# Optimization experiments

Measured on AMD Instinct MI355X. Metric: run time of the kernel, lower is better.

## Reference

```python
import jax, jax.numpy as jnp
import numpy as np

B, N, D = 2, 2048, 512
H, HD = 8, 64          # nheads, head_dim = D // H
RD = 16                # rl_dim
TEMPER = 1.0
BETA = 1.0
SLOPE = 0.01           # LeakyReLU negative slope
EPS = 1e-5             # LayerNorm eps


def setup_inputs() -> dict:
    key = jax.random.key(0)
    ks = jax.random.split(key, 12)
    s = 0.02
    return {
        "h": jax.random.normal(ks[0], (B, N, D), dtype=jnp.float32),
        "rh": jax.random.normal(ks[1], (B, N, RD), dtype=jnp.float32),
        # weights stored [in, out] (transpose of torch nn.Linear layout); y = x @ W
        "Wl": jax.random.normal(ks[2], (D, H * HD), dtype=jnp.float32) * s,
        "Wr": jax.random.normal(ks[3], (D, H * HD), dtype=jnp.float32) * s,
        "al": jax.random.normal(ks[4], (HD,), dtype=jnp.float32) * s,   # att_l weight
        "ar": jax.random.normal(ks[5], (HD,), dtype=jnp.float32) * s,   # att_r weight
        "Wrs": jax.random.normal(ks[6], (RD, H * RD), dtype=jnp.float32) * s,  # r_source
        "Wrt": jax.random.normal(ks[7], (RD, H * RD), dtype=jnp.float32) * s,  # r_target
        "Wf": jax.random.normal(ks[8], (H * HD, D), dtype=jnp.float32) * s,    # linear_final
        "gamma": jnp.ones((D,), dtype=jnp.float32),
        "beta": jnp.zeros((D,), dtype=jnp.float32),
    }


def _leaky(x):
    return jnp.where(x >= 0, x, SLOPE * x)


def reference(h, rh, Wl, Wr, al, ar, Wrs, Wrt, Wf, gamma, beta):
    # projections -> [B, H, N, HD]
    fl = (h @ Wl).reshape(B, N, H, HD).transpose(0, 2, 1, 3)
    fr = (h @ Wr).reshape(B, N, H, HD).transpose(0, 2, 1, 3)

    # additive GAT-style scores: [B,H,N,1] + [B,H,1,N] -> [B,H,N,N]
    sl = jnp.einsum("bhnd,d->bhn", _leaky(fl), al)
    sr = jnp.einsum("bhnd,d->bhn", _leaky(fr), ar)
    score = sl[:, :, :, None] + sr[:, :, None, :]

    # relational bias: r_k @ r_q -> [B,H,N,N]
    r_k = (rh @ Wrs).reshape(B, N, H, RD).transpose(0, 2, 1, 3)       # [B,H,N,RD]
    r_q = (rh @ Wrt).reshape(B, N, H, RD).transpose(0, 2, 3, 1)       # [B,H,RD,N]
    score = score + BETA * jnp.einsum("bhnr,bhrm->bhnm", r_k, r_q)

    attn = jax.nn.softmax(score / TEMPER, axis=-1)  # dropout1 is identity (eval)

    # weighted sum of fr (note: values are fr, not a separate V)
    context = jnp.einsum("bhnm,bhmd->bhnd", attn, fr)
    h_sa = context.transpose(0, 2, 1, 3).reshape(B, N, H * HD)
    fh = h_sa @ Wf                                   # dropout2 is identity (eval)

    # residual + LayerNorm
    x = h + fh
    mu = jnp.mean(x, axis=-1, keepdims=True)
    var = jnp.var(x, axis=-1, keepdims=True)
    return (x - mu) * jax.lax.rsqrt(var + EPS) * gamma + beta
```

## Files before the change

### kernel.cpp

```cpp
#include <hip/hip_runtime.h>
#include <hip/hip_bf16.h>

typedef __attribute__((ext_vector_type(8))) short short8;
typedef __attribute__((ext_vector_type(4))) float f32x4;
typedef __attribute__((ext_vector_type(4))) unsigned int u32x4;
typedef __attribute__((ext_vector_type(2))) unsigned int u32x2;

#define N_ 2048

__device__ __forceinline__ unsigned short f2bf(float f) {
  return __builtin_bit_cast(unsigned short, __float2bfloat16(f));
}
__device__ __forceinline__ float bf2f(unsigned short u) {
  return __builtin_bit_cast(float, ((unsigned int)u) << 16);
}
__device__ __forceinline__ unsigned int pack2(float lo, float hi) {
  return ((unsigned int)f2bf(hi) << 16) | (unsigned int)f2bf(lo);
}

__global__ __launch_bounds__(256) void k_cast_wT(const float* __restrict__ Wr,
                                                 const float* __restrict__ Wf,
                                                 unsigned short* __restrict__ WrT,
                                                 unsigned short* __restrict__ WfT) {
  const float* W = blockIdx.z ? Wf : Wr;
  unsigned short* WT = blockIdx.z ? WfT : WrT;
  __shared__ float t[32][33];
  const int kt = blockIdx.x * 32, ct = blockIdx.y * 32;
  const int r = threadIdx.x >> 3, c4 = (threadIdx.x & 7) * 4;
  f32x4 v = *reinterpret_cast<const f32x4*>(&W[(kt + r) * 512 + ct + c4]);
#pragma unroll
  for (int j = 0; j < 4; ++j) t[r][c4 + j] = v[j];
  __syncthreads();
  u32x2 o;
  o[0] = pack2(t[c4][r], t[c4 + 1][r]);
  o[1] = pack2(t[c4 + 2][r], t[c4 + 3][r]);
  *reinterpret_cast<u32x2*>(&WT[(ct + r) * 512 + kt + c4]) = o;
}

__global__ __launch_bounds__(256) void k_projr(
    const float* __restrict__ rh, const float* __restrict__ Wrs,
    const float* __restrict__ Wrt,
    unsigned short* __restrict__ rk, unsigned short* __restrict__ rq) {
  const int tid = threadIdx.x;
  const int col = tid & 127;
  const int ro = tid >> 7;
  const int nf = blockIdx.x * 2 + ro;
  const f32x4* src = reinterpret_cast<const f32x4*>(&rh[nf * 16]);
  f32x4 rv[4] = {src[0], src[1], src[2], src[3]};
  float sk = 0.f, sq = 0.f;
#pragma unroll
  for (int k4 = 0; k4 < 4; ++k4)
#pragma unroll
    for (int j = 0; j < 4; ++j) {
      float v = rv[k4][j];
      int k = k4 * 4 + j;
      sk += v * Wrs[k * 128 + col];
      sq += v * Wrt[k * 128 + col];
    }
  int bb = nf >> 11, n = nf & 2047, hh = col >> 4, r = col & 15;
  int oidx = ((bb * 8 + hh) * N_ + n) * 16 + r;
  rk[oidx] = f2bf(sk);
  rq[oidx] = f2bf(sq);
}

__global__ __launch_bounds__(256) void k_proj_fr(
    const float* __restrict__ h, const unsigned short* __restrict__ WrT,
    const float* __restrict__ ar,
    unsigned short* __restrict__ frB, float* __restrict__ sr) {
  const int tid = threadIdx.x;
  const int w = tid >> 6, lane = tid & 63;
  const int c = lane & 15, g = lane >> 4;
  const int rowbase = blockIdx.x * 16;
  const int hh = blockIdx.y * 4 + w;

  f32x4 acc[4];
#pragma unroll
  for (int i = 0; i < 4; ++i) acc[i] = (f32x4){0.f, 0.f, 0.f, 0.f};

#pragma unroll 4
  for (int kt = 0; kt < 512; kt += 32) {
    const float* hp = &h[(rowbase + c) * 512 + kt + 8 * g];
    f32x4 h0 = *reinterpret_cast<const f32x4*>(hp);
    f32x4 h1 = *reinterpret_cast<const f32x4*>(hp + 4);
    u32x4 aw;
    aw[0] = pack2(h0[0], h0[1]);
    aw[1] = pack2(h0[2], h0[3]);
    aw[2] = pack2(h1[0], h1[1]);
    aw[3] = pack2(h1[2], h1[3]);
    short8 a = __builtin_bit_cast(short8, aw);
#pragma unroll
    for (int ht = 0; ht < 4; ++ht) {
      short8 bv = *reinterpret_cast<const short8*>(
          &WrT[(hh * 64 + ht * 16 + c) * 512 + kt + 8 * g]);
      acc[ht] = __builtin_amdgcn_mfma_f32_16x16x32_bf16(a, bv, acc[ht], 0, 0, 0);
    }
  }

  const int b = rowbase >> 11;
  const int bh = b * 8 + hh;
  const int nloc = rowbase & 2047;
  const int jb = nloc >> 5;
  const int t = (nloc >> 4) & 1;

  float arv[4];
#pragma unroll
  for (int ht = 0; ht < 4; ++ht) arv[ht] = ar[ht * 16 + c];

  float ps[4];
#pragma unroll
  for (int r = 0; r < 4; ++r) {
    float s = 0.f;
#pragma unroll
    for (int ht = 0; ht < 4; ++ht) {
      float v = acc[ht][r];
      float lv = v >= 0.f ? v : 0.01f * v;
      s += lv * arv[ht];
    }
    ps[r] = s;
  }
#pragma unroll
  for (int msk = 1; msk < 16; msk <<= 1)
#pragma unroll
    for (int r = 0; r < 4; ++r) ps[r] += __shfl_xor(ps[r], msk);
  if (c == 0) {
#pragma unroll
    for (int r = 0; r < 4; ++r) sr[bh * N_ + nloc + 4 * g + r] = ps[r];
  }
#pragma unroll
  for (int ht = 0; ht < 4; ++ht) {
    int hd = ht * 16 + c;
    u32x2 ov;
    ov[0] = pack2(acc[ht][0], acc[ht][1]);
    ov[1] = pack2(acc[ht][2], acc[ht][3]);
    *reinterpret_cast<u32x2*>(
        &frB[((bh * 64 + jb) * 64 + hd) * 32 + 8 * g + 4 * t]) = ov;
  }
}

__global__ __launch_bounds__(128) void k_attn(
    const unsigned short* __restrict__ rk, const unsigned short* __restrict__ rq,
    const float* __restrict__ sr, const unsigned short* __restrict__ frB,
    unsigned short* __restrict__ O0, unsigned short* __restrict__ O1,
    unsigned short* __restrict__ O2, unsigned short* __restrict__ O3,
    float* __restrict__ lbuf) {
  const int tid = threadIdx.x;
  const int wave = tid >> 6, lane = tid & 63;
  const int c = lane & 15, g = lane >> 4;
  const int bh = blockIdx.y;
  const int b = bh >> 3, hh = bh & 7;
  const int z = blockIdx.z;
  const int qbase = blockIdx.x * 64 + wave * 32;

  short8 brk0 = {0, 0, 0, 0, 0, 0, 0, 0};
  short8 brk1 = {0, 0, 0, 0, 0, 0, 0, 0};
  if (g < 2) {
    brk0 = *reinterpret_cast<const short8*>(&rk[(bh * N_ + qbase + c) * 16 + 8 * g]);
    brk1 = *reinterpret_cast<const short8*>(&rk[(bh * N_ + qbase + 16 + c) * 16 + 8 * g]);
  } else if (g == 2) {
    brk0[0] = (short)0x3F80;
    brk1[0] = (short)0x3F80;
  }

  f32x4 O[2][4];
#pragma unroll
  for (int q = 0; q < 2; ++q)
#pragma unroll
    for (int i = 0; i < 4; ++i) O[q][i] = (f32x4){0.f, 0.f, 0.f, 0.f};
  float lacc0 = 0.f, lacc1 = 0.f;
  const unsigned short* frB_bh = frB + bh * 131072;

  for (int it = 0; it < 4; ++it) {
    const int j0 = z * 512 + it * 128;
    f32x4 S0[8], S1[8];
#pragma unroll
    for (int jh = 0; jh < 8; ++jh) {
      const int jr = j0 + jh * 16 + c;
      short8 a = {0, 0, 0, 0, 0, 0, 0, 0};
      if (g < 2)
        a = *reinterpret_cast<const short8*>(&rq[(bh * N_ + jr) * 16 + 8 * g]);
      else if (g == 2)
        a[0] = (short)f2bf(sr[bh * N_ + jr]);
      f32x4 zz = {0.f, 0.f, 0.f, 0.f};
      S0[jh] = __builtin_amdgcn_mfma_f32_16x16x32_bf16(a, brk0, zz, 0, 0, 0);
      S1[jh] = __builtin_amdgcn_mfma_f32_16x16x32_bf16(a, brk1, zz, 0, 0, 0);
    }
#pragma unroll
    for (int jh = 0; jh < 8; ++jh)
#pragma unroll
      for (int r = 0; r < 4; ++r) {
        float e0 = __expf(S0[jh][r]);
        S0[jh][r] = e0;
        lacc0 += e0;
        float e1 = __expf(S1[jh][r]);
        S1[jh][r] = e1;
        lacc1 += e1;
      }
#pragma unroll
    for (int kk = 0; kk < 4; ++kk) {
      u32x4 p0, p1;
      p0[0] = pack2(S0[2 * kk][0], S0[2 * kk][1]);
      p0[1] = pack2(S0[2 * kk][2], S0[2 * kk][3]);
      p0[2] = pack2(S0[2 * kk + 1][0], S0[2 * kk + 1][1]);
      p0[3] = pack2(S0[2 * kk + 1][2], S0[2 * kk + 1][3]);
      p1[0] = pack2(S1[2 * kk][0], S1[2 * kk][1]);
      p1[1] = pack2(S1[2 * kk][2], S1[2 * kk][3]);
      p1[2] = pack2(S1[2 * kk + 1][0], S1[2 * kk + 1][1]);
      p1[3] = pack2(S1[2 * kk + 1][2], S1[2 * kk + 1][3]);
      short8 pa0 = __builtin_bit_cast(short8, p0);
      short8 pa1 = __builtin_bit_cast(short8, p1);
      const int jb = (j0 >> 5) + kk;
      const unsigned short* fp = frB_bh + jb * 2048 + 8 * g;
#pragma unroll
      for (int ht = 0; ht < 4; ++ht) {
        short8 bv = *reinterpret_cast<const short8*>(fp + (ht * 16 + c) * 32);
        O[0][ht] = __builtin_amdgcn_mfma_f32_16x16x32_bf16(pa0, bv, O[0][ht], 0, 0, 0);
        O[1][ht] = __builtin_amdgcn_mfma_f32_16x16x32_bf16(pa1, bv, O[1][ht], 0, 0, 0);
      }
    }
  }
  lacc0 += __shfl_xor(lacc0, 16);
  lacc0 += __shfl_xor(lacc0, 32);
  lacc1 += __shfl_xor(lacc1, 16);
  lacc1 += __shfl_xor(lacc1, 32);
  if (g == 0) {
    lbuf[(z * 16 + bh) * N_ + qbase + c] = lacc0;
    lbuf[(z * 16 + bh) * N_ + qbase + 16 + c] = lacc1;
  }
  unsigned short* Oz = (z == 0) ? O0 : (z == 1) ? O1 : (z == 2) ? O2 : O3;
#pragma unroll
  for (int q = 0; q < 2; ++q)
#pragma unroll
    for (int ht = 0; ht < 4; ++ht)
#pragma unroll
      for (int r = 0; r < 4; ++r) {
        const int n = qbase + q * 16 + 4 * g + r;
        Oz[(b * N_ + n) * 512 + hh * 64 + ht * 16 + c] = f2bf(O[q][ht][r]);
      }
}

__global__ __launch_bounds__(256) void k_combine(
    const unsigned short* __restrict__ O0, const unsigned short* __restrict__ O1,
    const unsigned short* __restrict__ O2, const unsigned short* __restrict__ O3,
    const float* __restrict__ lbuf, unsigned short* __restrict__ ctx) {
  const int idx = blockIdx.x * 256 + threadIdx.x;
  const int row = idx >> 6;
  const int c8 = (idx & 63) * 8;
  const int b = row >> 11, n = row & 2047;
  const int hh = c8 >> 6;
  const int bh = b * 8 + hh;
  const float denom = lbuf[bh * N_ + n] + lbuf[(16 + bh) * N_ + n] +
                      lbuf[(32 + bh) * N_ + n] + lbuf[(48 + bh) * N_ + n];
  const float inv = 1.f / denom;
  const int off = row * 512 + c8;
  u32x4 v0 = *reinterpret_cast<const u32x4*>(&O0[off]);
  u32x4 v1 = *reinterpret_cast<const u32x4*>(&O1[off]);
  u32x4 v2 = *reinterpret_cast<const u32x4*>(&O2[off]);
  u32x4 v3 = *reinterpret_cast<const u32x4*>(&O3[off]);
  u32x4 ov;
#pragma unroll
  for (int j = 0; j < 4; ++j) {
    float lo = bf2f((unsigned short)(v0[j] & 0xffff)) + bf2f((unsigned short)(v1[j] & 0xffff)) +
               bf2f((unsigned short)(v2[j] & 0xffff)) + bf2f((unsigned short)(v3[j] & 0xffff));
    float hi = bf2f((unsigned short)(v0[j] >> 16)) + bf2f((unsigned short)(v1[j] >> 16)) +
               bf2f((unsigned short)(v2[j] >> 16)) + bf2f((unsigned short)(v3[j] >> 16));
    ov[j] = pack2(lo * inv, hi * inv);
  }
  *reinterpret_cast<u32x4*>(&ctx[off]) = ov;
}

__global__ __launch_bounds__(512) void k_final(
    const unsigned short* __restrict__ ctxB, const unsigned short* __restrict__ WfT,
    const float* __restrict__ h, const float* __restrict__ gamma,
    const float* __restrict__ beta, float* __restrict__ out) {
  __shared__ float red[2][16][9];
  __shared__ float mur[16], rsr[16];
  const int tid = threadIdx.x;
  const int w = tid >> 6, lane = tid & 63;
  const int c = lane & 15, g = lane >> 4;
  const int rowbase = blockIdx.x * 16;

  f32x4 acc[4];
#pragma unroll
  for (int i = 0; i < 4; ++i) acc[i] = (f32x4){0.f, 0.f, 0.f, 0.f};

#pragma unroll 4
  for (int kt = 0; kt < 512; kt += 32) {
    short8 a = *reinterpret_cast<const short8*>(&ctxB[(rowbase + c) * 512 + kt + 8 * g]);
#pragma unroll
    for (int ht = 0; ht < 4; ++ht) {
      short8 bv = *reinterpret_cast<const short8*>(
          &WfT[(w * 64 + ht * 16 + c) * 512 + kt + 8 * g]);
      acc[ht] = __builtin_amdgcn_mfma_f32_16x16x32_bf16(a, bv, acc[ht], 0, 0, 0);
    }
  }
  float x[4][4];
  float px[4], pxx[4];
#pragma unroll
  for (int r = 0; r < 4; ++r) { px[r] = 0.f; pxx[r] = 0.f; }
#pragma unroll
  for (int ht = 0; ht < 4; ++ht)
#pragma unroll
    for (int r = 0; r < 4; ++r) {
      float v = acc[ht][r] + h[(rowbase + 4 * g + r) * 512 + w * 64 + ht * 16 + c];
      x[ht][r] = v;
      px[r] += v;
      pxx[r] += v * v;
    }
#pragma unroll
  for (int msk = 1; msk < 16; msk <<= 1)
#pragma unroll
    for (int r = 0; r < 4; ++r) {
      px[r] += __shfl_xor(px[r], msk);
      pxx[r] += __shfl_xor(pxx[r], msk);
    }
  if (c == 0) {
#pragma unroll
    for (int r = 0; r < 4; ++r) {
      red[0][4 * g + r][w] = px[r];
      red[1][4 * g + r][w] = pxx[r];
    }
  }
  __syncthreads();
  if (tid < 16) {
    float s = 0.f, sq = 0.f;
#pragma unroll
    for (int wv = 0; wv < 8; ++wv) { s += red[0][tid][wv]; sq += red[1][tid][wv]; }
    float mu = s * (1.f / 512.f);
    float var = sq * (1.f / 512.f) - mu * mu;
    mur[tid] = mu;
    rsr[tid] = rsqrtf(var + 1e-5f);
  }
  __syncthreads();
#pragma unroll
  for (int ht = 0; ht < 4; ++ht)
#pragma unroll
    for (int r = 0; r < 4; ++r) {
      const int col = w * 64 + ht * 16 + c;
      const float mu = mur[4 * g + r], rs = rsr[4 * g + r];
      out[(rowbase + 4 * g + r) * 512 + col] =
          (x[ht][r] - mu) * rs * gamma[col] + beta[col];
    }
}

extern "C" void kernel_launch(void* const* d_in, const int* in_sizes, int n_in,
                              void* d_out, int out_size, void* d_ws, size_t ws_size,
                              hipStream_t stream) {
  const float* h     = (const float*)d_in[0];
  const float* rh    = (const float*)d_in[1];
  const float* Wr    = (const float*)d_in[3];
  const float* ar    = (const float*)d_in[5];
  const float* Wrs   = (const float*)d_in[6];
  const float* Wrt   = (const float*)d_in[7];
  const float* Wf    = (const float*)d_in[8];
  const float* gamma = (const float*)d_in[9];
  const float* beta  = (const float*)d_in[10];

  const size_t MB = 1ull << 20;
  char* ws = (char*)d_ws;
  unsigned short* frB  = (unsigned short*)(ws);
  unsigned short* rk   = (unsigned short*)(ws + 4 * MB);
  unsigned short* rq   = (unsigned short*)(ws + 5 * MB);
  float*          sr   = (float*)(ws + 6 * MB);
  float*          lbuf = (float*)(ws + 6 * MB + 256 * 1024);
  unsigned short* WrT  = (unsigned short*)(ws + 6 * MB + 768 * 1024);
  unsigned short* WfT  = (unsigned short*)(ws + 7 * MB + 256 * 1024);
  unsigned short* O0   = (unsigned short*)(ws + 7 * MB + 768 * 1024);
  unsigned short* O1   = (unsigned short*)(ws + 11 * MB + 768 * 1024);
  unsigned short* O2   = (unsigned short*)d_out;
  unsigned short* O3   = (unsigned short*)((char*)d_out + 4 * MB);

  hipLaunchKernelGGL(k_cast_wT, dim3(16, 16, 2), dim3(256), 0, stream, Wr, Wf, WrT, WfT);
  hipLaunchKernelGGL(k_projr, dim3(1024), dim3(256), 0, stream, rh, Wrs, Wrt, rk, rq);
  hipLaunchKernelGGL(k_proj_fr, dim3(256, 2), dim3(256), 0, stream, h, WrT, ar, frB, sr);
  hipLaunchKernelGGL(k_attn, dim3(32, 16, 4), dim3(128), 0, stream, rk, rq, sr, frB,
                     O0, O1, O2, O3, lbuf);
  hipLaunchKernelGGL(k_combine, dim3(1024), dim3(256), 0, stream, O0, O1, O2, O3, lbuf, frB);
  hipLaunchKernelGGL(k_final, dim3(256), dim3(512), 0, stream, frB, WfT, h, gamma, beta,
                     (float*)d_out);
}
```

Baseline: 185.8 us.

## Rewrite attention with 32x32x16 MFMA, permlane32 swaps, and merged prep kernel

The attention kernel now uses single-wave blocks with 32x32x16 bf16 MFMA for both the score and PV products. The sr bias is added in fp32 after the MFMA instead of being folded into the K dimension as a bf16 value, and the probabilities are rearranged into the B-operand layout with permlane32_swap. The fr buffer layout changes to 16-key tiles to match the new operand shape. Output stores become packed 32-bit writes per row. The weight-transpose and r-projection kernels are merged into one launch to save a kernel launch. The risks are lower occupancy from 64-thread blocks and more register pressure from the 16-wide accumulators.

```diff
diff --git a/kernel.cpp b/kernel.cpp
--- a/kernel.cpp
+++ b/kernel.cpp
@@ -3,8 +3,10 @@
 
 typedef __attribute__((ext_vector_type(8))) short short8;
 typedef __attribute__((ext_vector_type(4))) float f32x4;
+typedef __attribute__((ext_vector_type(16))) float f32x16;
 typedef __attribute__((ext_vector_type(4))) unsigned int u32x4;
 typedef __attribute__((ext_vector_type(2))) unsigned int u32x2;
+typedef __attribute__((ext_vector_type(2))) int i32x2;
 
 #define N_ 2048
 
@@ -18,55 +20,57 @@
   return ((unsigned int)f2bf(hi) << 16) | (unsigned int)f2bf(lo);
 }
 
-__global__ __launch_bounds__(256) void k_cast_wT(const float* __restrict__ Wr,
-                                                 const float* __restrict__ Wf,
-                                                 unsigned short* __restrict__ WrT,
-                                                 unsigned short* __restrict__ WfT) {
-  const float* W = blockIdx.z ? Wf : Wr;
-  unsigned short* WT = blockIdx.z ? WfT : WrT;
-  __shared__ float t[32][33];
-  const int kt = blockIdx.x * 32, ct = blockIdx.y * 32;
-  const int r = threadIdx.x >> 3, c4 = (threadIdx.x & 7) * 4;
-  f32x4 v = *reinterpret_cast<const f32x4*>(&W[(kt + r) * 512 + ct + c4]);
-#pragma unroll
-  for (int j = 0; j < 4; ++j) t[r][c4 + j] = v[j];
-  __syncthreads();
-  u32x2 o;
-  o[0] = pack2(t[c4][r], t[c4 + 1][r]);
-  o[1] = pack2(t[c4 + 2][r], t[c4 + 3][r]);
-  *reinterpret_cast<u32x2*>(&WT[(ct + r) * 512 + kt + c4]) = o;
-}
-
-__global__ __launch_bounds__(256) void k_projr(
+__global__ __launch_bounds__(256) void k_prep(
+    const float* __restrict__ Wr, const float* __restrict__ Wf,
     const float* __restrict__ rh, const float* __restrict__ Wrs,
     const float* __restrict__ Wrt,
+    unsigned short* __restrict__ WrT, unsigned short* __restrict__ WfT,
     unsigned short* __restrict__ rk, unsigned short* __restrict__ rq) {
+  __shared__ float t[32][33];
+  const int bid = blockIdx.x;
   const int tid = threadIdx.x;
-  const int col = tid & 127;
-  const int ro = tid >> 7;
-  const int nf = blockIdx.x * 2 + ro;
-  const f32x4* src = reinterpret_cast<const f32x4*>(&rh[nf * 16]);
-  f32x4 rv[4] = {src[0], src[1], src[2], src[3]};
-  float sk = 0.f, sq = 0.f;
-#pragma unroll
-  for (int k4 = 0; k4 < 4; ++k4)
-#pragma unroll
-    for (int j = 0; j < 4; ++j) {
-      float v = rv[k4][j];
-      int k = k4 * 4 + j;
-      sk += v * Wrs[k * 128 + col];
-      sq += v * Wrt[k * 128 + col];
-    }
-  int bb = nf >> 11, n = nf & 2047, hh = col >> 4, r = col & 15;
-  int oidx = ((bb * 8 + hh) * N_ + n) * 16 + r;
-  rk[oidx] = f2bf(sk);
-  rq[oidx] = f2bf(sq);
+  if (bid < 512) {
+    const int zz = bid >> 8, rem = bid & 255;
+    const int kt = (rem & 15) * 32, ct = (rem >> 4) * 32;
+    const float* W = zz ? Wf : Wr;
+    unsigned short* WT = zz ? WfT : WrT;
+    const int r = tid >> 3, c4 = (tid & 7) * 4;
+    f32x4 v = *reinterpret_cast<const f32x4*>(&W[(kt + r) * 512 + ct + c4]);
+#pragma unroll
+    for (int j = 0; j < 4; ++j) t[r][c4 + j] = v[j];
+    __syncthreads();
+    u32x2 o;
+    o[0] = pack2(t[c4][r], t[c4 + 1][r]);
+    o[1] = pack2(t[c4 + 2][r], t[c4 + 3][r]);
+    *reinterpret_cast<u32x2*>(&WT[(ct + r) * 512 + kt + c4]) = o;
+  } else {
+    const int pb = bid - 512;
+    const int col = tid & 127;
+    const int ro = tid >> 7;
+    const int nf = pb * 2 + ro;
+    const f32x4* src = reinterpret_cast<const f32x4*>(&rh[nf * 16]);
+    f32x4 rv[4] = {src[0], src[1], src[2], src[3]};
+    float sk = 0.f, sq = 0.f;
+#pragma unroll
+    for (int k4 = 0; k4 < 4; ++k4)
+#pragma unroll
+      for (int j = 0; j < 4; ++j) {
+        float v = rv[k4][j];
+        int k = k4 * 4 + j;
+        sk += v * Wrs[k * 128 + col];
+        sq += v * Wrt[k * 128 + col];
+      }
+    int bb = nf >> 11, n = nf & 2047, hh = col >> 4, r = col & 15;
+    int oidx = ((bb * 8 + hh) * N_ + n) * 16 + r;
+    rk[oidx] = f2bf(sk);
+    rq[oidx] = f2bf(sq);
+  }
 }
 
 __global__ __launch_bounds__(256) void k_proj_fr(
     const float* __restrict__ h, const unsigned short* __restrict__ WrT,
     const float* __restrict__ ar,
-    unsigned short* __restrict__ frB, float* __restrict__ sr) {
+    unsigned short* __restrict__ frBt, float* __restrict__ sr) {
   const int tid = threadIdx.x;
   const int w = tid >> 6, lane = tid & 63;
   const int c = lane & 15, g = lane >> 4;
@@ -99,8 +103,7 @@
   const int b = rowbase >> 11;
   const int bh = b * 8 + hh;
   const int nloc = rowbase & 2047;
-  const int jb = nloc >> 5;
-  const int t = (nloc >> 4) & 1;
+  const int jb = nloc >> 4;
 
   float arv[4];
 #pragma unroll
@@ -133,109 +136,96 @@
     ov[0] = pack2(acc[ht][0], acc[ht][1]);
     ov[1] = pack2(acc[ht][2], acc[ht][3]);
     *reinterpret_cast<u32x2*>(
-        &frB[((bh * 64 + jb) * 64 + hd) * 32 + 8 * g + 4 * t]) = ov;
-  }
-}
-
-__global__ __launch_bounds__(128) void k_attn(
+        &frBt[(((size_t)bh * 128 + jb) * 64 + hd) * 16 + 4 * g]) = ov;
+  }
+}
+
+__global__ __launch_bounds__(64) void k_attn(
     const unsigned short* __restrict__ rk, const unsigned short* __restrict__ rq,
-    const float* __restrict__ sr, const unsigned short* __restrict__ frB,
+    const float* __restrict__ sr, const unsigned short* __restrict__ frBt,
     unsigned short* __restrict__ O0, unsigned short* __restrict__ O1,
     unsigned short* __restrict__ O2, unsigned short* __restrict__ O3,
     float* __restrict__ lbuf) {
-  const int tid = threadIdx.x;
-  const int wave = tid >> 6, lane = tid & 63;
-  const int c = lane & 15, g = lane >> 4;
-  const int bh = blockIdx.y;
-  const int b = bh >> 3, hh = bh & 7;
+  const int lane = threadIdx.x;
+  const int c5 = lane & 31, hi = lane >> 5;
+  const int bh = blockIdx.y, b = bh >> 3, hh = bh & 7;
   const int z = blockIdx.z;
-  const int qbase = blockIdx.x * 64 + wave * 32;
-
-  short8 brk0 = {0, 0, 0, 0, 0, 0, 0, 0};
-  short8 brk1 = {0, 0, 0, 0, 0, 0, 0, 0};
-  if (g < 2) {
-    brk0 = *reinterpret_cast<const short8*>(&rk[(bh * N_ + qbase + c) * 16 + 8 * g]);
-    brk1 = *reinterpret_cast<const short8*>(&rk[(bh * N_ + qbase + 16 + c) * 16 + 8 * g]);
-  } else if (g == 2) {
-    brk0[0] = (short)0x3F80;
-    brk1[0] = (short)0x3F80;
-  }
-
-  f32x4 O[2][4];
-#pragma unroll
-  for (int q = 0; q < 2; ++q)
-#pragma unroll
-    for (int i = 0; i < 4; ++i) O[q][i] = (f32x4){0.f, 0.f, 0.f, 0.f};
-  float lacc0 = 0.f, lacc1 = 0.f;
-  const unsigned short* frB_bh = frB + bh * 131072;
+  const int qbase = blockIdx.x * 32;
+
+  const short8 brk =
+      *reinterpret_cast<const short8*>(&rk[(bh * N_ + qbase + c5) * 16 + 8 * hi]);
+
+  f32x16 Oa = {0.f, 0.f, 0.f, 0.f, 0.f, 0.f, 0.f, 0.f,
+               0.f, 0.f, 0.f, 0.f, 0.f, 0.f, 0.f, 0.f};
+  f32x16 Ob = Oa;
+  float l = 0.f;
+  const float* sr_bh = sr + bh * N_;
+  const unsigned short* rq_bh = rq + (size_t)bh * N_ * 16;
+  const unsigned short* fb = frBt + (size_t)bh * 128 * 64 * 16;
 
   for (int it = 0; it < 4; ++it) {
     const int j0 = z * 512 + it * 128;
-    f32x4 S0[8], S1[8];
-#pragma unroll
-    for (int jh = 0; jh < 8; ++jh) {
-      const int jr = j0 + jh * 16 + c;
-      short8 a = {0, 0, 0, 0, 0, 0, 0, 0};
-      if (g < 2)
-        a = *reinterpret_cast<const short8*>(&rq[(bh * N_ + jr) * 16 + 8 * g]);
-      else if (g == 2)
-        a[0] = (short)f2bf(sr[bh * N_ + jr]);
-      f32x4 zz = {0.f, 0.f, 0.f, 0.f};
-      S0[jh] = __builtin_amdgcn_mfma_f32_16x16x32_bf16(a, brk0, zz, 0, 0, 0);
-      S1[jh] = __builtin_amdgcn_mfma_f32_16x16x32_bf16(a, brk1, zz, 0, 0, 0);
-    }
-#pragma unroll
-    for (int jh = 0; jh < 8; ++jh)
-#pragma unroll
-      for (int r = 0; r < 4; ++r) {
-        float e0 = __expf(S0[jh][r]);
-        S0[jh][r] = e0;
-        lacc0 += e0;
-        float e1 = __expf(S1[jh][r]);
-        S1[jh][r] = e1;
-        lacc1 += e1;
-      }
-#pragma unroll
-    for (int kk = 0; kk < 4; ++kk) {
-      u32x4 p0, p1;
-      p0[0] = pack2(S0[2 * kk][0], S0[2 * kk][1]);
-      p0[1] = pack2(S0[2 * kk][2], S0[2 * kk][3]);
-      p0[2] = pack2(S0[2 * kk + 1][0], S0[2 * kk + 1][1]);
-      p0[3] = pack2(S0[2 * kk + 1][2], S0[2 * kk + 1][3]);
-      p1[0] = pack2(S1[2 * kk][0], S1[2 * kk][1]);
-      p1[1] = pack2(S1[2 * kk][2], S1[2 * kk][3]);
-      p1[2] = pack2(S1[2 * kk + 1][0], S1[2 * kk + 1][1]);
-      p1[3] = pack2(S1[2 * kk + 1][2], S1[2 * kk + 1][3]);
-      short8 pa0 = __builtin_bit_cast(short8, p0);
-      short8 pa1 = __builtin_bit_cast(short8, p1);
-      const int jb = (j0 >> 5) + kk;
-      const unsigned short* fp = frB_bh + jb * 2048 + 8 * g;
-#pragma unroll
-      for (int ht = 0; ht < 4; ++ht) {
-        short8 bv = *reinterpret_cast<const short8*>(fp + (ht * 16 + c) * 32);
-        O[0][ht] = __builtin_amdgcn_mfma_f32_16x16x32_bf16(pa0, bv, O[0][ht], 0, 0, 0);
-        O[1][ht] = __builtin_amdgcn_mfma_f32_16x16x32_bf16(pa1, bv, O[1][ht], 0, 0, 0);
-      }
-    }
-  }
-  lacc0 += __shfl_xor(lacc0, 16);
-  lacc0 += __shfl_xor(lacc0, 32);
-  lacc1 += __shfl_xor(lacc1, 16);
-  lacc1 += __shfl_xor(lacc1, 32);
-  if (g == 0) {
-    lbuf[(z * 16 + bh) * N_ + qbase + c] = lacc0;
-    lbuf[(z * 16 + bh) * N_ + qbase + 16 + c] = lacc1;
-  }
+#pragma unroll
+    for (int t = 0; t < 4; ++t) {
+      const int jb = j0 + t * 32;
+      short8 a = *reinterpret_cast<const short8*>(&rq_bh[(jb + c5) * 16 + 8 * hi]);
+      f32x16 zz = {0.f, 0.f, 0.f, 0.f, 0.f, 0.f, 0.f, 0.f,
+                   0.f, 0.f, 0.f, 0.f, 0.f, 0.f, 0.f, 0.f};
+      f32x16 S = __builtin_amdgcn_mfma_f32_32x32x16_bf16(a, brk, zz, 0, 0, 0);
+      f32x4 sa = *reinterpret_cast<const f32x4*>(&sr_bh[jb + 4 * hi]);
+      f32x4 sb = *reinterpret_cast<const f32x4*>(&sr_bh[jb + 8 + 4 * hi]);
+      f32x4 sc = *reinterpret_cast<const f32x4*>(&sr_bh[jb + 16 + 4 * hi]);
+      f32x4 sd = *reinterpret_cast<const f32x4*>(&sr_bh[jb + 24 + 4 * hi]);
+      float p[16];
+#pragma unroll
+      for (int r = 0; r < 4; ++r) p[r] = __expf(S[r] + sa[r]);
+#pragma unroll
+      for (int r = 0; r < 4; ++r) p[4 + r] = __expf(S[4 + r] + sb[r]);
+#pragma unroll
+      for (int r = 0; r < 4; ++r) p[8 + r] = __expf(S[8 + r] + sc[r]);
+#pragma unroll
+      for (int r = 0; r < 4; ++r) p[12 + r] = __expf(S[12 + r] + sd[r]);
+#pragma unroll
+      for (int r = 0; r < 16; ++r) l += p[r];
+      int A1 = (int)pack2(p[0], p[1]), B1 = (int)pack2(p[2], p[3]);
+      int C1 = (int)pack2(p[4], p[5]), D1 = (int)pack2(p[6], p[7]);
+      i32x2 r0 = __builtin_amdgcn_permlane32_swap(A1, C1, false, false);
+      i32x2 r1 = __builtin_amdgcn_permlane32_swap(B1, D1, false, false);
+      int A2 = (int)pack2(p[8], p[9]), B2 = (int)pack2(p[10], p[11]);
+      int C2 = (int)pack2(p[12], p[13]), D2 = (int)pack2(p[14], p[15]);
+      i32x2 r2 = __builtin_amdgcn_permlane32_swap(A2, C2, false, false);
+      i32x2 r3 = __builtin_amdgcn_permlane32_swap(B2, D2, false, false);
+      u32x4 f1, f2;
+      f1[0] = (unsigned)r0[0]; f1[1] = (unsigned)r1[0];
+      f1[2] = (unsigned)r0[1]; f1[3] = (unsigned)r1[1];
+      f2[0] = (unsigned)r2[0]; f2[1] = (unsigned)r3[0];
+      f2[2] = (unsigned)r2[1]; f2[3] = (unsigned)r3[1];
+      short8 pb1 = __builtin_bit_cast(short8, f1);
+      short8 pb2 = __builtin_bit_cast(short8, f2);
+      const unsigned short* fp0 = fb + ((size_t)(jb >> 4) * 64) * 16 + 8 * hi;
+      const unsigned short* fp1 = fp0 + 64 * 16;
+      short8 av;
+      av = *reinterpret_cast<const short8*>(fp0 + c5 * 16);
+      Oa = __builtin_amdgcn_mfma_f32_32x32x16_bf16(av, pb1, Oa, 0, 0, 0);
+      av = *reinterpret_cast<const short8*>(fp0 + (32 + c5) * 16);
+      Ob = __builtin_amdgcn_mfma_f32_32x32x16_bf16(av, pb1, Ob, 0, 0, 0);
+      av = *reinterpret_cast<const short8*>(fp1 + c5 * 16);
+      Oa = __builtin_amdgcn_mfma_f32_32x32x16_bf16(av, pb2, Oa, 0, 0, 0);
+      av = *reinterpret_cast<const short8*>(fp1 + (32 + c5) * 16);
+      Ob = __builtin_amdgcn_mfma_f32_32x32x16_bf16(av, pb2, Ob, 0, 0, 0);
+    }
+  }
+  l += __shfl_xor(l, 32);
+  if (hi == 0) lbuf[(z * 16 + bh) * N_ + qbase + c5] = l;
   unsigned short* Oz = (z == 0) ? O0 : (z == 1) ? O1 : (z == 2) ? O2 : O3;
-#pragma unroll
-  for (int q = 0; q < 2; ++q)
-#pragma unroll
-    for (int ht = 0; ht < 4; ++ht)
-#pragma unroll
-      for (int r = 0; r < 4; ++r) {
-        const int n = qbase + q * 16 + 4 * g + r;
-        Oz[(b * N_ + n) * 512 + hh * 64 + ht * 16 + c] = f2bf(O[q][ht][r]);
-      }
+  unsigned int* orow = reinterpret_cast<unsigned int*>(
+      &Oz[((size_t)(b * N_ + qbase + c5)) * 512 + hh * 64]);
+#pragma unroll
+  for (int r = 0; r < 16; r += 2) {
+    const int hd = (r & 3) + 8 * (r >> 2) + 4 * hi;
+    orow[hd >> 1] = pack2(Oa[r], Oa[r + 1]);
+    orow[(32 + hd) >> 1] = pack2(Ob[r], Ob[r + 1]);
+  }
 }
 
 __global__ __launch_bounds__(256) void k_combine(
@@ -357,7 +347,7 @@
 
   const size_t MB = 1ull << 20;
   char* ws = (char*)d_ws;
-  unsigned short* frB  = (unsigned short*)(ws);
+  unsigned short* frBt = (unsigned short*)(ws);
   unsigned short* rk   = (unsigned short*)(ws + 4 * MB);
   unsigned short* rq   = (unsigned short*)(ws + 5 * MB);
   float*          sr   = (float*)(ws + 6 * MB);
@@ -369,12 +359,12 @@
   unsigned short* O2   = (unsigned short*)d_out;
   unsigned short* O3   = (unsigned short*)((char*)d_out + 4 * MB);
 
-  hipLaunchKernelGGL(k_cast_wT, dim3(16, 16, 2), dim3(256), 0, stream, Wr, Wf, WrT, WfT);
-  hipLaunchKernelGGL(k_projr, dim3(1024), dim3(256), 0, stream, rh, Wrs, Wrt, rk, rq);
-  hipLaunchKernelGGL(k_proj_fr, dim3(256, 2), dim3(256), 0, stream, h, WrT, ar, frB, sr);
-  hipLaunchKernelGGL(k_attn, dim3(32, 16, 4), dim3(128), 0, stream, rk, rq, sr, frB,
+  hipLaunchKernelGGL(k_prep, dim3(2560), dim3(256), 0, stream,
+                     Wr, Wf, rh, Wrs, Wrt, WrT, WfT, rk, rq);
+  hipLaunchKernelGGL(k_proj_fr, dim3(256, 2), dim3(256), 0, stream, h, WrT, ar, frBt, sr);
+  hipLaunchKernelGGL(k_attn, dim3(64, 16, 4), dim3(64), 0, stream, rk, rq, sr, frBt,
                      O0, O1, O2, O3, lbuf);
-  hipLaunchKernelGGL(k_combine, dim3(1024), dim3(256), 0, stream, O0, O1, O2, O3, lbuf, frB);
-  hipLaunchKernelGGL(k_final, dim3(256), dim3(512), 0, stream, frB, WfT, h, gamma, beta,
+  hipLaunchKernelGGL(k_combine, dim3(1024), dim3(256), 0, stream, O0, O1, O2, O3, lbuf, frBt);
+  hipLaunchKernelGGL(k_final, dim3(256), dim3(512), 0, stream, frBt, WfT, h, gamma, beta,
                      (float*)d_out);
 }
```

After: 175.7 us. 1.06x faster.
